# Performance work log

Hardware: AMD Instinct MI355X
Metric: run time of the kernel (lower is better)

The kernel has to match this reference:

```python
import jax, jax.numpy as jnp
import numpy as np

IMG_B, IMG_H, IMG_W, IMG_C = 16, 512, 1024, 3

def _base_grid(B, H, W):
    # replicates the module's custom normalization: arange/dim * 2 - 1
    base_x = (jnp.arange(W, dtype=jnp.float32) / W) * 2.0 - 1.0   # [W]
    base_y = (jnp.arange(H, dtype=jnp.float32) / H) * 2.0 - 1.0   # [H]
    base = jnp.stack([jnp.broadcast_to(base_x[None, :], (H, W)),
                      jnp.broadcast_to(base_y[:, None], (H, W))], axis=-1)  # [H,W,2]
    return jnp.broadcast_to(base[None], (B, H, W, 2))

def _grid_sample_bilinear_zeros(im, grid):
    # im: [B,C,H,W], grid: [B,Ho,Wo,2] in [-1,1], align_corners=False, zeros padding
    B, C, H, W = im.shape
    gx, gy = grid[..., 0], grid[..., 1]
    ix = ((gx + 1.0) * W - 1.0) * 0.5
    iy = ((gy + 1.0) * H - 1.0) * 0.5
    x0 = jnp.floor(ix); y0 = jnp.floor(iy)
    wx1 = ix - x0; wx0 = 1.0 - wx1
    wy1 = iy - y0; wy0 = 1.0 - wy1
    x0i = x0.astype(jnp.int32); y0i = y0.astype(jnp.int32)
    b_idx = jnp.arange(B, dtype=jnp.int32)[:, None, None]

    def corner(xi, yi, w):
        valid = (xi >= 0) & (xi < W) & (yi >= 0) & (yi < H)
        xc = jnp.clip(xi, 0, W - 1); yc = jnp.clip(yi, 0, H - 1)
        # advanced indexing -> [B,Ho,Wo,C]
        v = im[b_idx, :, yc, xc]
        return v * (w * valid.astype(im.dtype))[..., None]

    out = (corner(x0i,     y0i,     wx0 * wy0) +
           corner(x0i + 1, y0i,     wx1 * wy0) +
           corner(x0i,     y0i + 1, wx0 * wy1) +
           corner(x0i + 1, y0i + 1, wx1 * wy1))           # [B,Ho,Wo,C]
    return jnp.transpose(out, (0, 3, 1, 2))                # [B,C,Ho,Wo]

def setup_inputs() -> dict:
    key = jax.random.key(0)
    k1, k2, k3 = jax.random.split(key, 3)
    pred_flow = jax.random.normal(k1, (IMG_B, IMG_H, IMG_W, 2), dtype=jnp.float32) * 8.0
    im1_origin = jax.random.uniform(k2, (IMG_B, IMG_C, IMG_H, IMG_W), dtype=jnp.float32)
    im2_origin = jax.random.uniform(k3, (IMG_B, IMG_C, IMG_H, IMG_W), dtype=jnp.float32)
    return {"pred_flow": pred_flow, "im1_origin": im1_origin, "im2_origin": im2_origin}

def reference(pred_flow, im1_origin, im2_origin):
    B, H, W, _ = pred_flow.shape
    scale = jnp.array([W, H], dtype=pred_flow.dtype)
    grid = pred_flow / scale + _base_grid(B, H, W)
    im1_warp = _grid_sample_bilinear_zeros(im1_origin, grid)
    loss = jnp.sum(jnp.abs(im2_origin - im1_warp)) / (W * H)
    return loss
```

## Files before the change

### kernel.cpp

```cpp
#include <hip/hip_runtime.h>

namespace {

constexpr int B = 16, C = 3, H = 512, W = 1024;
constexpr int HW = H * W;
constexpr int SLABW = 256, SLABH = 128;
constexpr int XH  = 16;
constexpr int SWD = SLABW + 2 * XH;
constexpr int PADW = SWD + 5;
constexpr int RING = 32;
constexpr int RA = 11;
constexpr int RB = 16;
constexpr int RPS = 4;
constexpr int BLOCK = 1024;
constexpr int TX = W / SLABW;
constexpr int TY = H / SLABH;
constexpr int GRID = B * TX * TY;
constexpr int PF_ROWS = RA + RB + 1;
constexpr int STG_N = C * RPS * SWD;

constexpr float INV_W = 1.0f / 1024.0f;
constexpr float INV_H = 1.0f / 512.0f;

__device__ __forceinline__ float2 ld2g(const float* p) {
    struct __attribute__((packed, aligned(4))) F2 { float a, b; };
    const F2 v = *reinterpret_cast<const F2*>(p);
    return make_float2(v.a, v.b);
}

__global__ __launch_bounds__(BLOCK, 4) void flow_loss_partial(
    const float* __restrict__ flow,
    const float* __restrict__ im1,
    const float* __restrict__ im2,
    float* __restrict__ partials)
{
    __shared__ float smem[C * RING * PADW];
    __shared__ float red[BLOCK / 64];

    const int tid = threadIdx.x;
    const int bid = blockIdx.x;
    const int b   = bid >> 4;
    const int tt  = bid & 15;
    const int tyi = tt >> 2;
    const int txi = tt & 3;
    const int xbase  = txi * SLABW;
    const int yStart = tyi * SLABH;

    const float* __restrict__ im1b = im1 + b * C * HW;
    const float* __restrict__ im2b = im2 + b * C * HW;
    const float* __restrict__ flb  = flow + 2 * (b * HW);

    for (int e = tid; e < PF_ROWS * C * SWD; e += BLOCK) {
        const int scol = e % SWD;
        const int rc   = e / SWD;
        const int c    = rc / PF_ROWS;
        const int ri   = rc - c * PF_ROWS;
        const int row  = yStart - RA + ri;
        if (row >= 0) {
            const int gcol = min(max(xbase - XH + scol, 0), W - 1);
            smem[(c * RING + (row & (RING - 1))) * PADW + scol] =
                im1b[c * HW + row * W + gcol];
        }
    }

    int  stSr[4], stGBase[4], stLBase[4];
    bool stOK[4];
#pragma unroll
    for (int k = 0; k < 4; ++k) {
        const int e = k * BLOCK + tid;
        stOK[k] = (e < STG_N);
        const int ec   = stOK[k] ? e : 0;
        const int scol = ec % SWD;
        const int rc   = ec / SWD;
        const int c    = rc >> 2;
        stSr[k]   = rc & 3;
        const int gcol = min(max(xbase - XH + scol, 0), W - 1);
        stGBase[k] = c * HW + gcol;
        stLBase[k] = (c * RING) * PADW + scol;
    }

    auto issue = [&](int r0, int (&sIdx)[4], float (&sVal)[4]) {
#pragma unroll
        for (int k = 0; k < 4; ++k) {
            const int srow = r0 + stSr[k];
            int idx = -1; float v = 0.0f;
            if (stOK[k] & (srow < H)) {
                v   = im1b[stGBase[k] + (srow << 10)];
                idx = stLBase[k] + (srow & (RING - 1)) * PADW;
            }
            sIdx[k] = idx; sVal[k] = v;
        }
    };

    int   sIA[4]; float sVA[4];
    issue(yStart + RB + 1, sIA, sVA);

    __syncthreads();

    const int colp = tid & (SLABW - 1);
    const int prow = tid >> 8;
    const int x = xbase + colp;
    const float base_x = (float)x * (2.0f * INV_W) - 1.0f;

    float acc = 0.0f;

#pragma unroll 1
    for (int ys = yStart; ys < yStart + SLABH; ys += RPS) {
        int   sIB[4]; float sVB[4];
        issue(ys + RB + 1 + RPS, sIB, sVB);

        const int y = ys + prow;
        const float2 f = *reinterpret_cast<const float2*>(flb + 2 * (y * W + x));

        const float base_y = (float)y * (2.0f * INV_H) - 1.0f;
        const float gx = __builtin_fmaf(f.x, INV_W, base_x);
        const float gy = __builtin_fmaf(f.y, INV_H, base_y);
        const float ixf = __builtin_fmaf(gx + 1.0f, 512.0f, -0.5f);
        const float iyf = __builtin_fmaf(gy + 1.0f, 256.0f, -0.5f);

        const float x0f = floorf(ixf), y0f = floorf(iyf);
        const float wx1 = ixf - x0f, wx0 = 1.0f - wx1;
        const float wy1 = iyf - y0f, wy0 = 1.0f - wy1;
        const int x0 = (int)x0f, y0 = (int)y0f;
        const int x1 = x0 + 1,   y1 = y0 + 1;
        const bool vx0 = (x0 >= 0) & (x0 < W);
        const bool vx1 = (x1 >= 0) & (x1 < W);
        const bool vy0 = (y0 >= 0) & (y0 < H);
        const bool vy1 = (y1 >= 0) & (y1 < H);
        const float w00 = wx0 * wy0 * (float)(vx0 & vy0);
        const float w01 = wx1 * wy0 * (float)(vx1 & vy0);
        const float w10 = wx0 * wy1 * (float)(vx0 & vy1);
        const float w11 = wx1 * wy1 * (float)(vx1 & vy1);
        const int xL  = min(max(x0, 0), W - 2);
        const int x0c = min(max(x0, 0), W - 1);
        const int x1c = min(max(x1, 0), W - 1);
        const int y0c = min(max(y0, 0), H - 1);
        const int y1c = min(max(y1, 0), H - 1);
        const bool s0 = (x0c != xL), s1 = (x1c != xL);
        const float aT0 = (s0 ? 0.0f : w00) + (s1 ? 0.0f : w01);
        const float aT1 = (s0 ? w00 : 0.0f) + (s1 ? w01 : 0.0f);
        const float aB0 = (s0 ? 0.0f : w10) + (s1 ? 0.0f : w11);
        const float aB1 = (s0 ? w10 : 0.0f) + (s1 ? w11 : 0.0f);

        const int jj = xL - xbase + XH;
        const bool inR = (y0c >= ys - RA) & (y1c <= ys + RB) &
                         ((unsigned)jj <= (unsigned)(SWD - 2));

        const int zoff = y * W + x;
        const float z0 = im2b[zoff];
        const float z1 = im2b[HW + zoff];
        const float z2 = im2b[2 * HW + zoff];

        float wp0, wp1, wp2;
        if (inR) {
            const int lT = (y0c & (RING - 1)) * PADW + jj;
            const int lB = (y1c & (RING - 1)) * PADW + jj;
            const float t00 = smem[lT],                   t01 = smem[lT + 1];
            const float b00 = smem[lB],                   b01 = smem[lB + 1];
            const float t10 = smem[RING * PADW + lT],     t11 = smem[RING * PADW + lT + 1];
            const float b10 = smem[RING * PADW + lB],     b11 = smem[RING * PADW + lB + 1];
            const float t20 = smem[2 * RING * PADW + lT], t21 = smem[2 * RING * PADW + lT + 1];
            const float b20 = smem[2 * RING * PADW + lB], b21 = smem[2 * RING * PADW + lB + 1];
            wp0 = ((aT0 * t00 + aT1 * t01) + aB0 * b00) + aB1 * b01;
            wp1 = ((aT0 * t10 + aT1 * t11) + aB0 * b10) + aB1 * b11;
            wp2 = ((aT0 * t20 + aT1 * t21) + aB0 * b20) + aB1 * b21;
        } else {
            const int oT = y0c * W + xL, oB = y1c * W + xL;
            const float2 ta = ld2g(im1b + oT),            ba = ld2g(im1b + oB);
            const float2 tb = ld2g(im1b + HW + oT),       bb = ld2g(im1b + HW + oB);
            const float2 tc = ld2g(im1b + 2 * HW + oT),   bc = ld2g(im1b + 2 * HW + oB);
            wp0 = ((aT0 * ta.x + aT1 * ta.y) + aB0 * ba.x) + aB1 * ba.y;
            wp1 = ((aT0 * tb.x + aT1 * tb.y) + aB0 * bb.x) + aB1 * bb.y;
            wp2 = ((aT0 * tc.x + aT1 * tc.y) + aB0 * bc.x) + aB1 * bc.y;
        }
        acc += fabsf(z0 - wp0) + fabsf(z1 - wp1) + fabsf(z2 - wp2);

#pragma unroll
        for (int k = 0; k < 4; ++k)
            if (sIA[k] >= 0) smem[sIA[k]] = sVA[k];
        __syncthreads();

#pragma unroll
        for (int k = 0; k < 4; ++k) { sIA[k] = sIB[k]; sVA[k] = sVB[k]; }
    }

#pragma unroll
    for (int o = 32; o > 0; o >>= 1)
        acc += __shfl_down(acc, o, 64);
    const int lane = tid & 63;
    const int wid  = tid >> 6;
    if (lane == 0) red[wid] = acc;
    __syncthreads();
    if (tid == 0) {
        float s = 0.0f;
#pragma unroll
        for (int wv = 0; wv < BLOCK / 64; ++wv) s += red[wv];
        partials[bid] = s;
    }
}

__global__ __launch_bounds__(256) void flow_loss_reduce(
    const float* __restrict__ partials, float* __restrict__ out)
{
    __shared__ double lds[256];
    double s = 0.0;
    for (int i = threadIdx.x; i < 256; i += 256) {}
    double acc = 0.0;
    for (int i = threadIdx.x; i < GRID; i += 256) acc += (double)partials[i];
    lds[threadIdx.x] = acc;
    __syncthreads();
    for (int o = 128; o > 0; o >>= 1) {
        if (threadIdx.x < o) lds[threadIdx.x] += lds[threadIdx.x + o];
        __syncthreads();
    }
    if (threadIdx.x == 0) out[0] = (float)(lds[0] / (double)(W * H));
    (void)s;
}

}

extern "C" void kernel_launch(void* const* d_in, const int* in_sizes, int n_in,
                              void* d_out, int out_size, void* d_ws, size_t ws_size,
                              hipStream_t stream) {
    const float* flow = (const float*)d_in[0];
    const float* im1  = (const float*)d_in[1];
    const float* im2  = (const float*)d_in[2];
    float* out = (float*)d_out;
    float* partials = (float*)d_ws;

    flow_loss_partial<<<GRID, BLOCK, 0, stream>>>(flow, im1, im2, partials);
    flow_loss_reduce<<<1, 256, 0, stream>>>(partials, out);
}
```

Measured before the change: 64.60 us.

## Store im1 ring buffer as packed fp16 pairs and halve slab height

The LDS ring buffer holding im1 rows now stores pairs of pixels packed as fp16 in 32-bit words, roughly halving LDS footprint. Bilinear taps are recovered with a funnel-shift to handle odd alignment. Slab height is halved to double the block count, and launch bounds now request 8 blocks per CU for higher occupancy. The trade-off is fp16 rounding of image values in the interpolation, which changes numerics slightly, plus extra halo prefetch work per output row.

New measurement: 60.32 us. 6.6% less time.

```diff
diff --git a/kernel.cpp b/kernel.cpp
--- a/kernel.cpp
+++ b/kernel.cpp
@@ -1,13 +1,15 @@
 #include <hip/hip_runtime.h>
+#include <hip/hip_fp16.h>
 
 namespace {
 
 constexpr int B = 16, C = 3, H = 512, W = 1024;
 constexpr int HW = H * W;
-constexpr int SLABW = 256, SLABH = 128;
+constexpr int SLABW = 256, SLABH = 64;
 constexpr int XH  = 16;
 constexpr int SWD = SLABW + 2 * XH;
-constexpr int PADW = SWD + 5;
+constexpr int PAIRS = SWD / 2;
+constexpr int PADP = 147;
 constexpr int RING = 32;
 constexpr int RA = 11;
 constexpr int RB = 16;
@@ -17,7 +19,8 @@
 constexpr int TY = H / SLABH;
 constexpr int GRID = B * TX * TY;
 constexpr int PF_ROWS = RA + RB + 1;
-constexpr int STG_N = C * RPS * SWD;
+constexpr int STG_P = C * RPS * PAIRS;
+constexpr int CHS = RING * PADP;
 
 constexpr float INV_W = 1.0f / 1024.0f;
 constexpr float INV_H = 1.0f / 512.0f;
@@ -28,89 +31,109 @@
     return make_float2(v.a, v.b);
 }
 
-__global__ __launch_bounds__(BLOCK, 4) void flow_loss_partial(
+__device__ __forceinline__ uint32_t packh2(float a, float b) {
+    return (uint32_t)__half_as_ushort(__float2half_rn(a))
+         | ((uint32_t)__half_as_ushort(__float2half_rn(b)) << 16);
+}
+__device__ __forceinline__ float2 unpackh2(uint32_t u) {
+    const __half2 h = __builtin_bit_cast(__half2, u);
+    return make_float2(__low2float(h), __high2float(h));
+}
+__device__ __forceinline__ uint32_t alignsel(uint32_t hi, uint32_t lo, int sh) {
+    return (uint32_t)(((((uint64_t)hi) << 32) | (uint64_t)lo) >> sh);
+}
+
+__global__ __launch_bounds__(BLOCK, 8) void flow_loss_partial(
     const float* __restrict__ flow,
     const float* __restrict__ im1,
     const float* __restrict__ im2,
     float* __restrict__ partials)
 {
-    __shared__ float smem[C * RING * PADW];
+    __shared__ uint32_t sm32[C * CHS];
     __shared__ float red[BLOCK / 64];
 
     const int tid = threadIdx.x;
     const int bid = blockIdx.x;
-    const int b   = bid >> 4;
-    const int tt  = bid & 15;
+    const int b   = bid >> 5;
+    const int tt  = bid & 31;
     const int tyi = tt >> 2;
     const int txi = tt & 3;
     const int xbase  = txi * SLABW;
     const int yStart = tyi * SLABH;
+    const int xb0    = xbase - XH;
 
     const float* __restrict__ im1b = im1 + b * C * HW;
     const float* __restrict__ im2b = im2 + b * C * HW;
     const float* __restrict__ flb  = flow + 2 * (b * HW);
 
-    for (int e = tid; e < PF_ROWS * C * SWD; e += BLOCK) {
-        const int scol = e % SWD;
-        const int rc   = e / SWD;
-        const int c    = rc / PF_ROWS;
-        const int ri   = rc - c * PF_ROWS;
-        const int row  = yStart - RA + ri;
+    for (int e = tid; e < PF_ROWS * C * PAIRS; e += BLOCK) {
+        const int q  = e % PAIRS;
+        const int rc = e / PAIRS;
+        const int c  = rc / PF_ROWS;
+        const int ri = rc - c * PF_ROWS;
+        const int row = yStart - RA + ri;
         if (row >= 0) {
-            const int gcol = min(max(xbase - XH + scol, 0), W - 1);
-            smem[(c * RING + (row & (RING - 1))) * PADW + scol] =
-                im1b[c * HW + row * W + gcol];
+            const int g0 = min(max(xb0 + 2 * q, 0), W - 1);
+            const int g1 = min(max(xb0 + 2 * q + 1, 0), W - 1);
+            const float a = im1b[c * HW + row * W + g0];
+            const float d = im1b[c * HW + row * W + g1];
+            sm32[c * CHS + (row & (RING - 1)) * PADP + q] = packh2(a, d);
         }
     }
 
-    int  stSr[4], stGBase[4], stLBase[4];
-    bool stOK[4];
-#pragma unroll
-    for (int k = 0; k < 4; ++k) {
+    int  stSr[2], stG0[2], stG1[2], stL[2];
+    bool stOK[2];
+#pragma unroll
+    for (int k = 0; k < 2; ++k) {
         const int e = k * BLOCK + tid;
-        stOK[k] = (e < STG_N);
-        const int ec   = stOK[k] ? e : 0;
-        const int scol = ec % SWD;
-        const int rc   = ec / SWD;
-        const int c    = rc >> 2;
-        stSr[k]   = rc & 3;
-        const int gcol = min(max(xbase - XH + scol, 0), W - 1);
-        stGBase[k] = c * HW + gcol;
-        stLBase[k] = (c * RING) * PADW + scol;
-    }
-
-    auto issue = [&](int r0, int (&sIdx)[4], float (&sVal)[4]) {
-#pragma unroll
-        for (int k = 0; k < 4; ++k) {
+        stOK[k] = (e < STG_P);
+        const int ec = stOK[k] ? e : 0;
+        const int q  = ec % PAIRS;
+        const int rc = ec / PAIRS;
+        const int c  = rc >> 2;
+        stSr[k] = rc & 3;
+        const int g0 = min(max(xb0 + 2 * q, 0), W - 1);
+        const int g1 = min(max(xb0 + 2 * q + 1, 0), W - 1);
+        stG0[k] = c * HW + g0;
+        stG1[k] = c * HW + g1;
+        stL[k]  = c * CHS + q;
+    }
+
+    auto issue = [&](int r0, int (&sIdx)[2], uint32_t (&sVal)[2]) {
+#pragma unroll
+        for (int k = 0; k < 2; ++k) {
             const int srow = r0 + stSr[k];
-            int idx = -1; float v = 0.0f;
+            int idx = -1; uint32_t v = 0;
             if (stOK[k] & (srow < H)) {
-                v   = im1b[stGBase[k] + (srow << 10)];
-                idx = stLBase[k] + (srow & (RING - 1)) * PADW;
+                const float a = im1b[stG0[k] + (srow << 10)];
+                const float d = im1b[stG1[k] + (srow << 10)];
+                v   = packh2(a, d);
+                idx = stL[k] + (srow & (RING - 1)) * PADP;
             }
             sIdx[k] = idx; sVal[k] = v;
         }
     };
 
-    int   sIA[4]; float sVA[4];
+    int sIA[2]; uint32_t sVA[2];
     issue(yStart + RB + 1, sIA, sVA);
-
-    __syncthreads();
 
     const int colp = tid & (SLABW - 1);
     const int prow = tid >> 8;
     const int x = xbase + colp;
     const float base_x = (float)x * (2.0f * INV_W) - 1.0f;
 
+    __syncthreads();
+
     float acc = 0.0f;
 
 #pragma unroll 1
     for (int ys = yStart; ys < yStart + SLABH; ys += RPS) {
-        int   sIB[4]; float sVB[4];
+        int sIB[2]; uint32_t sVB[2];
         issue(ys + RB + 1 + RPS, sIB, sVB);
 
         const int y = ys + prow;
-        const float2 f = *reinterpret_cast<const float2*>(flb + 2 * (y * W + x));
+        const int zoff = y * W + x;
+        const float2 f = *reinterpret_cast<const float2*>(flb + 2 * zoff);
 
         const float base_y = (float)y * (2.0f * INV_H) - 1.0f;
         const float gx = __builtin_fmaf(f.x, INV_W, base_x);
@@ -146,24 +169,31 @@
         const bool inR = (y0c >= ys - RA) & (y1c <= ys + RB) &
                          ((unsigned)jj <= (unsigned)(SWD - 2));
 
-        const int zoff = y * W + x;
         const float z0 = im2b[zoff];
         const float z1 = im2b[HW + zoff];
         const float z2 = im2b[2 * HW + zoff];
 
         float wp0, wp1, wp2;
         if (inR) {
-            const int lT = (y0c & (RING - 1)) * PADW + jj;
-            const int lB = (y1c & (RING - 1)) * PADW + jj;
-            const float t00 = smem[lT],                   t01 = smem[lT + 1];
-            const float b00 = smem[lB],                   b01 = smem[lB + 1];
-            const float t10 = smem[RING * PADW + lT],     t11 = smem[RING * PADW + lT + 1];
-            const float b10 = smem[RING * PADW + lB],     b11 = smem[RING * PADW + lB + 1];
-            const float t20 = smem[2 * RING * PADW + lT], t21 = smem[2 * RING * PADW + lT + 1];
-            const float b20 = smem[2 * RING * PADW + lB], b21 = smem[2 * RING * PADW + lB + 1];
-            wp0 = ((aT0 * t00 + aT1 * t01) + aB0 * b00) + aB1 * b01;
-            wp1 = ((aT0 * t10 + aT1 * t11) + aB0 * b10) + aB1 * b11;
-            wp2 = ((aT0 * t20 + aT1 * t21) + aB0 * b20) + aB1 * b21;
+            const int q  = jj >> 1;
+            const int sh = (jj & 1) << 4;
+            const int aT = (y0c & (RING - 1)) * PADP + q;
+            const int aB = (y1c & (RING - 1)) * PADP + q;
+            const uint32_t dT0a = sm32[aT],           dT0b = sm32[aT + 1];
+            const uint32_t dB0a = sm32[aB],           dB0b = sm32[aB + 1];
+            const uint32_t dT1a = sm32[aT + CHS],     dT1b = sm32[aT + CHS + 1];
+            const uint32_t dB1a = sm32[aB + CHS],     dB1b = sm32[aB + CHS + 1];
+            const uint32_t dT2a = sm32[aT + 2 * CHS], dT2b = sm32[aT + 2 * CHS + 1];
+            const uint32_t dB2a = sm32[aB + 2 * CHS], dB2b = sm32[aB + 2 * CHS + 1];
+            const float2 t0 = unpackh2(alignsel(dT0b, dT0a, sh));
+            const float2 b0 = unpackh2(alignsel(dB0b, dB0a, sh));
+            const float2 t1 = unpackh2(alignsel(dT1b, dT1a, sh));
+            const float2 b1 = unpackh2(alignsel(dB1b, dB1a, sh));
+            const float2 t2 = unpackh2(alignsel(dT2b, dT2a, sh));
+            const float2 b2 = unpackh2(alignsel(dB2b, dB2a, sh));
+            wp0 = ((aT0 * t0.x + aT1 * t0.y) + aB0 * b0.x) + aB1 * b0.y;
+            wp1 = ((aT0 * t1.x + aT1 * t1.y) + aB0 * b1.x) + aB1 * b1.y;
+            wp2 = ((aT0 * t2.x + aT1 * t2.y) + aB0 * b2.x) + aB1 * b2.y;
         } else {
             const int oT = y0c * W + xL, oB = y1c * W + xL;
             const float2 ta = ld2g(im1b + oT),            ba = ld2g(im1b + oB);
@@ -176,12 +206,12 @@
         acc += fabsf(z0 - wp0) + fabsf(z1 - wp1) + fabsf(z2 - wp2);
 
 #pragma unroll
-        for (int k = 0; k < 4; ++k)
-            if (sIA[k] >= 0) smem[sIA[k]] = sVA[k];
+        for (int k = 0; k < 2; ++k)
+            if (sIA[k] >= 0) sm32[sIA[k]] = sVA[k];
         __syncthreads();
 
 #pragma unroll
-        for (int k = 0; k < 4; ++k) { sIA[k] = sIB[k]; sVA[k] = sVB[k]; }
+        for (int k = 0; k < 2; ++k) { sIA[k] = sIB[k]; sVA[k] = sVB[k]; }
     }
 
 #pragma unroll
@@ -203,8 +233,6 @@
     const float* __restrict__ partials, float* __restrict__ out)
 {
     __shared__ double lds[256];
-    double s = 0.0;
-    for (int i = threadIdx.x; i < 256; i += 256) {}
     double acc = 0.0;
     for (int i = threadIdx.x; i < GRID; i += 256) acc += (double)partials[i];
     lds[threadIdx.x] = acc;
@@ -214,7 +242,6 @@
         __syncthreads();
     }
     if (threadIdx.x == 0) out[0] = (float)(lds[0] / (double)(W * H));
-    (void)s;
 }
 
 }
```
